# Optimization experiments

Hardware: AMD Instinct MI355X
Metric: run time of the kernel (lower is better)

The kernel has to match this reference:

```python
import jax, jax.numpy as jnp
import numpy as np

# module hyperparameters (from init_kwargs)
STRIDE, PAD, DIL = 1, 1, 1
GROUPS, DG = 1, 1
KH, KW = 3, 3
CIN, COUT = 256, 256


def _mdcn_forward(x, offset, mask, weight, bias):
    B, C, H, W = x.shape
    Cout = weight.shape[0]
    K = KH * KW
    Ho = (H + 2 * PAD - (DIL * (KH - 1) + 1)) // STRIDE + 1
    Wo = (W + 2 * PAD - (DIL * (KW - 1) + 1)) // STRIDE + 1
    Cg = C // DG

    # offset channel layout: ((g*K + k)*2 + {0: dy, 1: dx})
    off = offset.reshape(B, DG, KH, KW, 2, Ho, Wo)
    base_y = (jnp.arange(Ho) * STRIDE - PAD)[None, :] + DIL * jnp.arange(KH)[:, None]  # [KH,Ho]
    base_x = (jnp.arange(Wo) * STRIDE - PAD)[None, :] + DIL * jnp.arange(KW)[:, None]  # [KW,Wo]
    sy = base_y[None, None, :, None, :, None].astype(x.dtype) + off[:, :, :, :, 0]  # [B,DG,KH,KW,Ho,Wo]
    sx = base_x[None, None, None, :, None, :].astype(x.dtype) + off[:, :, :, :, 1]

    y0f = jnp.floor(sy); x0f = jnp.floor(sx)
    wy = sy - y0f; wx = sx - x0f
    y0 = y0f.astype(jnp.int32); x0 = x0f.astype(jnp.int32)

    xg = x.reshape(B, DG, Cg, H * W)

    def corner(yc, xc, w):
        valid = (yc >= 0) & (yc < H) & (xc >= 0) & (xc < W)
        idx = jnp.clip(yc, 0, H - 1) * W + jnp.clip(xc, 0, W - 1)  # [B,DG,KH,KW,Ho,Wo]
        v = jnp.take_along_axis(xg, idx.reshape(B, DG, 1, -1), axis=3)  # [B,DG,Cg,K*Ho*Wo]
        v = v.reshape(B, DG, Cg, KH, KW, Ho, Wo)
        return v * (w * valid.astype(x.dtype))[:, :, None]

    val = (corner(y0, x0, (1 - wy) * (1 - wx))
           + corner(y0, x0 + 1, (1 - wy) * wx)
           + corner(y0 + 1, x0, wy * (1 - wx))
           + corner(y0 + 1, x0 + 1, wy * wx))  # [B,DG,Cg,KH,KW,Ho,Wo]

    cols = val * mask.reshape(B, DG, 1, KH, KW, Ho, Wo)
    cols = cols.reshape(B, GROUPS, (C // GROUPS) * K, Ho * Wo)
    wg = weight.reshape(GROUPS, Cout // GROUPS, (C // GROUPS) * K)
    out = jnp.einsum('gok,bgkp->bgop', wg, cols).reshape(B, Cout, Ho, Wo)
    return out + bias[None, :, None, None]


def setup_inputs() -> dict:
    key = jax.random.key(0)
    k1, k2, k3, k4 = jax.random.split(key, 4)
    B, H, W = 4, 64, 64
    x = jax.random.normal(k1, (B, CIN, H, W), dtype=jnp.float32)
    offset = jax.random.normal(k2, (B, 2 * DG * KH * KW, H, W), dtype=jnp.float32)
    mask = jax.random.uniform(k3, (B, DG * KH * KW, H, W), dtype=jnp.float32)
    stdv = 1.0 / np.sqrt(CIN * KH * KW)
    weight = jax.random.uniform(k4, (COUT, CIN // GROUPS, KH, KW), dtype=jnp.float32,
                                minval=-stdv, maxval=stdv)
    bias = jnp.zeros((COUT,), dtype=jnp.float32)
    return {"x": x, "offset": offset, "mask": mask, "weight": weight, "bias": bias}


def reference(x, offset, mask, weight, bias):
    return _mdcn_forward(x, offset, mask, weight, bias)
```

## Files before the change

kernel.cpp:

```cpp
#include <hip/hip_runtime.h>
#include <hip/hip_bf16.h>
#include <stdint.h>

#define KDIM 2304

typedef __bf16 bf16_t;
typedef bf16_t bf16x8 __attribute__((ext_vector_type(8)));
typedef float f32x4 __attribute__((ext_vector_type(4)));
typedef float f32x2 __attribute__((ext_vector_type(2)));

__device__ __forceinline__ float b2f_lo(uint32_t u) {
  union { uint32_t i; float f; } c; c.i = u << 16; return c.f;
}
__device__ __forceinline__ float b2f_hi(uint32_t u) {
  union { uint32_t i; float f; } c; c.i = u & 0xffff0000u; return c.f;
}
__device__ __forceinline__ uint32_t pk_bf16(float a, float b) {
  __hip_bfloat162 h = __float22bfloat162_rn(make_float2(a, b));
  union { __hip_bfloat162 h; uint32_t u; } c; c.h = h; return c.u;
}

__device__ __forceinline__ void g2lds16(const uint16_t* g, uint16_t* l) {
  __builtin_amdgcn_global_load_lds((const __attribute__((address_space(1))) void*)g,
                                   (__attribute__((address_space(3))) void*)l,
                                   16, 0, 0);
}

__global__ __launch_bounds__(256) void k_transpose(const float* __restrict__ x,
                                                   uint16_t* __restrict__ xt) {
  __shared__ float tile[32][33];
  int b = blockIdx.z;
  int c0 = blockIdx.y << 5;
  int s0 = blockIdx.x << 5;
  int tid = threadIdx.x;
  int tx = tid & 31, ty = tid >> 5;
  const float* src = x + ((size_t)(b * 256 + c0)) * 4096 + s0;
#pragma unroll
  for (int i = 0; i < 4; ++i)
    tile[ty + i * 8][tx] = src[(size_t)(ty + i * 8) * 4096 + tx];
  __syncthreads();
  int cg = tid & 7, sp = tid >> 3;
  uint2 o;
  o.x = pk_bf16(tile[cg * 4 + 0][sp], tile[cg * 4 + 1][sp]);
  o.y = pk_bf16(tile[cg * 4 + 2][sp], tile[cg * 4 + 3][sp]);
  *(uint2*)&xt[((size_t)b * 4096 + s0 + sp) * 256 + c0 + cg * 4] = o;
}

__global__ __launch_bounds__(256) void k_wprep(const float* __restrict__ w,
                                               uint16_t* __restrict__ wt) {
  int t = blockIdx.x * 256 + threadIdx.x;
  int cout = t / KDIM;
  int r = t - cout * KDIM;
  int k = r >> 8, c = r & 255;
  wt[t] = (uint16_t)(pk_bf16(w[((size_t)(cout * 256 + c)) * 9 + k], 0.f) & 0xffffu);
}

__global__ __launch_bounds__(256) void k_im2col(const uint16_t* __restrict__ xt,
                                                const float* __restrict__ off,
                                                const float* __restrict__ msk,
                                                uint16_t* __restrict__ cols) {
  __shared__ float s_off[18 * 16];
  __shared__ float s_msk[9 * 16];
  int blk = blockIdx.x;
  int wq = blk & 3;
  int ho = (blk >> 2) & 63;
  int b = blk >> 8;
  int w0 = wq << 4;
  int tid = threadIdx.x;
  if (tid < 18 * 16) {
    int ch = tid >> 4, woi = tid & 15;
    s_off[tid] = off[((size_t)(b * 18 + ch)) * 4096 + ho * 64 + w0 + woi];
  } else if (tid >= 64 && tid < 64 + 9 * 16) {
    int i = tid - 64;
  }
  __syncthreads();
  for (int i = tid; i < 18 * 16; i += 256) {
    int ch = i >> 4, woi = i & 15;
    s_off[i] = off[((size_t)(b * 18 + ch)) * 4096 + ho * 64 + w0 + woi];
  }
  for (int i = tid; i < 9 * 16; i += 256) {
    int ch = i >> 4, woi = i & 15;
    s_msk[i] = msk[((size_t)(b * 9 + ch)) * 4096 + ho * 64 + w0 + woi];
  }
  __syncthreads();
  int wv = tid >> 6, lane = tid & 63;
  int half = lane >> 5, li = lane & 31;
  int c8 = li << 3;
  const uint16_t* base = xt + (size_t)b * 4096 * 256;
  uint16_t* cbase = cols + ((size_t)b * 4096 + (size_t)ho * 64 + w0) * KDIM;
  for (int p = wv; p < 72; p += 4) {
    int s = 2 * p + half;
    int k = s >> 4, woi = s & 15;
    int kh = k / 3, kw = k - kh * 3;
    float dy = s_off[(2 * k) * 16 + woi];
    float dx = s_off[(2 * k + 1) * 16 + woi];
    float mm = s_msk[k * 16 + woi];
    float sy = (float)(ho - 1 + kh) + dy;
    float sx = (float)(w0 + woi - 1 + kw) + dx;
    float fy = floorf(sy), fx = floorf(sx);
    int y0 = (int)fy, x0 = (int)fx;
    float wy = sy - fy, wx = sx - fx;
    f32x2 a0 = {0.f, 0.f}, a1 = {0.f, 0.f}, a2 = {0.f, 0.f}, a3 = {0.f, 0.f};
#pragma unroll
    for (int cy = 0; cy < 2; ++cy) {
#pragma unroll
      for (int cx = 0; cx < 2; ++cx) {
        int y = y0 + cy, x = x0 + cx;
        float w = (cy ? wy : 1.f - wy) * (cx ? wx : 1.f - wx);
        bool v = ((unsigned)y < 64u) && ((unsigned)x < 64u);
        w = v ? w : 0.f;
        int yc = min(max(y, 0), 63), xc = min(max(x, 0), 63);
        const uint4 d = *(const uint4*)(base + (((size_t)yc * 64 + xc) * 256 + c8));
        f32x2 ww = {w, w};
        a0 += ww * f32x2{b2f_lo(d.x), b2f_hi(d.x)};
        a1 += ww * f32x2{b2f_lo(d.y), b2f_hi(d.y)};
        a2 += ww * f32x2{b2f_lo(d.z), b2f_hi(d.z)};
        a3 += ww * f32x2{b2f_lo(d.w), b2f_hi(d.w)};
      }
    }
    f32x2 mm2 = {mm, mm};
    a0 *= mm2; a1 *= mm2; a2 *= mm2; a3 *= mm2;
    uint4 o;
    o.x = pk_bf16(a0.x, a0.y);
    o.y = pk_bf16(a1.x, a1.y);
    o.z = pk_bf16(a2.x, a2.y);
    o.w = pk_bf16(a3.x, a3.y);
    *(uint4*)(cbase + (size_t)woi * KDIM + k * 256 + c8) = o;
  }
}

#define BM 128
#define BN 64
#define BK 32
__global__ __launch_bounds__(256) void k_gemm(const uint16_t* __restrict__ A,
                                              const uint16_t* __restrict__ Bm,
                                              const float* __restrict__ bias,
                                              float* __restrict__ out) {
  __shared__ __align__(16) uint16_t As[BM * BK];
  __shared__ __align__(16) uint16_t Bs[BN * BK];
  int tid = threadIdx.x;
  int lane = tid & 63, wv = tid >> 6;
  int wm = wv >> 1, wn = wv & 1;
  int m0 = blockIdx.y * BM, n0 = blockIdx.x * BN;
  int q = lane >> 4, r = lane & 15;

  f32x4 acc[4][2];
#pragma unroll
  for (int i = 0; i < 4; ++i)
#pragma unroll
    for (int j = 0; j < 2; ++j) acc[i][j] = f32x4{0.f, 0.f, 0.f, 0.f};

  const uint16_t* a0p = A + (size_t)(m0 + (tid >> 2)) * KDIM + (tid & 3) * 8;
  const uint16_t* a1p = A + (size_t)(m0 + 64 + (tid >> 2)) * KDIM + (tid & 3) * 8;
  const uint16_t* b0p = Bm + (size_t)(n0 + (tid >> 2)) * KDIM + (tid & 3) * 8;
  uint16_t* as0 = &As[tid * 8];
  uint16_t* as1 = &As[2048 + tid * 8];
  uint16_t* bs0 = &Bs[tid * 8];

  for (int k0 = 0; k0 < KDIM; k0 += BK) {
    g2lds16(a0p + k0, as0);
    g2lds16(a1p + k0, as1);
    g2lds16(b0p + k0, bs0);
    __syncthreads();
    bf16x8 af[4], bfr[2];
#pragma unroll
    for (int mi = 0; mi < 4; ++mi)
      af[mi] = *(const bf16x8*)&As[(wm * 64 + mi * 16 + r) * BK + q * 8];
#pragma unroll
    for (int ni = 0; ni < 2; ++ni)
      bfr[ni] = *(const bf16x8*)&Bs[(wn * 32 + ni * 16 + r) * BK + q * 8];
#pragma unroll
    for (int mi = 0; mi < 4; ++mi)
#pragma unroll
      for (int ni = 0; ni < 2; ++ni)
        acc[mi][ni] = __builtin_amdgcn_mfma_f32_16x16x32_bf16(af[mi], bfr[ni], acc[mi][ni], 0, 0, 0);
    __syncthreads();
  }

#pragma unroll
  for (int mi = 0; mi < 4; ++mi) {
#pragma unroll
    for (int j = 0; j < 4; ++j) {
      int m = m0 + wm * 64 + mi * 16 + q * 4 + j;
      float bv = bias[m];
#pragma unroll
      for (int ni = 0; ni < 2; ++ni) {
        int n = n0 + wn * 32 + ni * 16 + r;
        int b = n >> 12, p = n & 4095;
        out[((size_t)(b * 256 + m)) * 4096 + p] = acc[mi][ni][j] + bv;
      }
    }
  }
}

extern "C" void kernel_launch(void* const* d_in, const int* in_sizes, int n_in,
                              void* d_out, int out_size, void* d_ws, size_t ws_size,
                              hipStream_t stream) {
  (void)in_sizes; (void)n_in; (void)out_size; (void)ws_size;
  const float* x      = (const float*)d_in[0];
  const float* offset = (const float*)d_in[1];
  const float* mask   = (const float*)d_in[2];
  const float* weight = (const float*)d_in[3];
  const float* bias   = (const float*)d_in[4];
  float* out = (float*)d_out;

  uint8_t* ws = (uint8_t*)d_ws;
  uint16_t* xt   = (uint16_t*)ws;
  uint16_t* wt   = (uint16_t*)(ws + 8388608);
  uint16_t* cols = (uint16_t*)(ws + 9568256);

  k_transpose<<<dim3(128, 8, 4), 256, 0, stream>>>(x, xt);
  k_wprep<<<dim3(2304), 256, 0, stream>>>(weight, wt);
  k_im2col<<<dim3(1024), 256, 0, stream>>>(xt, offset, mask, cols);
  k_gemm<<<dim3(256, 2), 256, 0, stream>>>(wt, cols, bias, out);
}
```

Before: 141.4 us.

## Fuse deformable im2col sampling into the GEMM B-tile loader

Removes the separate im2col kernel and its large bf16 cols buffer in global memory. Each GEMM block now computes its B tile on the fly by bilinearly sampling the channel-last input for one tap and 32 channels per K-step, with the mask folded into the corner weights. This trades the cols write and re-read traffic for redundant sampling, since each of the two M-blocks recomputes the same B tiles. It also puts gather latency inside the MFMA loop with no double buffering.

```diff
diff --git a/kernel.cpp b/kernel.cpp
--- a/kernel.cpp
+++ b/kernel.cpp
@@ -55,126 +55,127 @@
   wt[t] = (uint16_t)(pk_bf16(w[((size_t)(cout * 256 + c)) * 9 + k], 0.f) & 0xffffu);
 }
 
-__global__ __launch_bounds__(256) void k_im2col(const uint16_t* __restrict__ xt,
-                                                const float* __restrict__ off,
-                                                const float* __restrict__ msk,
-                                                uint16_t* __restrict__ cols) {
-  __shared__ float s_off[18 * 16];
-  __shared__ float s_msk[9 * 16];
-  int blk = blockIdx.x;
-  int wq = blk & 3;
-  int ho = (blk >> 2) & 63;
-  int b = blk >> 8;
-  int w0 = wq << 4;
+#define BM 128
+#define BN 64
+#define BK 32
+__global__ __launch_bounds__(256) void k_fused(const uint16_t* __restrict__ xt,
+                                               const uint16_t* __restrict__ A,
+                                               const float* __restrict__ off,
+                                               const float* __restrict__ msk,
+                                               const float* __restrict__ bias,
+                                               float* __restrict__ out) {
+  __shared__ __align__(16) uint16_t As[BM * BK];
+  __shared__ __align__(16) uint16_t Bs[BN * BK];
+  __shared__ float s_off[18 * 64];
+  __shared__ float s_msk[9 * 64];
+
   int tid = threadIdx.x;
-  if (tid < 18 * 16) {
-    int ch = tid >> 4, woi = tid & 15;
-    s_off[tid] = off[((size_t)(b * 18 + ch)) * 4096 + ho * 64 + w0 + woi];
-  } else if (tid >= 64 && tid < 64 + 9 * 16) {
-    int i = tid - 64;
-  }
+  int n0 = blockIdx.x << 6;
+  int m0 = blockIdx.y << 7;
+  int b = blockIdx.x >> 6;
+  int ho = blockIdx.x & 63;
+
+  const float* offb = off + (size_t)b * 18 * 4096 + ho * 64;
+  for (int i = tid; i < 18 * 64; i += 256)
+    s_off[i] = offb[(size_t)(i >> 6) * 4096 + (i & 63)];
+  const float* mskb = msk + (size_t)b * 9 * 4096 + ho * 64;
+  for (int i = tid; i < 9 * 64; i += 256)
+    s_msk[i] = mskb[(size_t)(i >> 6) * 4096 + (i & 63)];
   __syncthreads();
-  for (int i = tid; i < 18 * 16; i += 256) {
-    int ch = i >> 4, woi = i & 15;
-    s_off[i] = off[((size_t)(b * 18 + ch)) * 4096 + ho * 64 + w0 + woi];
-  }
-  for (int i = tid; i < 9 * 16; i += 256) {
-    int ch = i >> 4, woi = i & 15;
-    s_msk[i] = msk[((size_t)(b * 9 + ch)) * 4096 + ho * 64 + w0 + woi];
-  }
-  __syncthreads();
-  int wv = tid >> 6, lane = tid & 63;
-  int half = lane >> 5, li = lane & 31;
-  int c8 = li << 3;
-  const uint16_t* base = xt + (size_t)b * 4096 * 256;
-  uint16_t* cbase = cols + ((size_t)b * 4096 + (size_t)ho * 64 + w0) * KDIM;
-  for (int p = wv; p < 72; p += 4) {
-    int s = 2 * p + half;
-    int k = s >> 4, woi = s & 15;
-    int kh = k / 3, kw = k - kh * 3;
-    float dy = s_off[(2 * k) * 16 + woi];
-    float dx = s_off[(2 * k + 1) * 16 + woi];
-    float mm = s_msk[k * 16 + woi];
+
+  int lane = tid & 63, wv = tid >> 6;
+  int wm = wv >> 1, wn = wv & 1;
+  int q = lane >> 4, r = lane & 15;
+
+  f32x4 acc[4][2];
+#pragma unroll
+  for (int i = 0; i < 4; ++i)
+#pragma unroll
+    for (int j = 0; j < 2; ++j) acc[i][j] = f32x4{0.f, 0.f, 0.f, 0.f};
+
+  const uint16_t* a0p = A + (size_t)(m0 + (tid >> 2)) * KDIM + (tid & 3) * 8;
+  const uint16_t* a1p = A + (size_t)(m0 + 64 + (tid >> 2)) * KDIM + (tid & 3) * 8;
+  uint16_t* as0 = &As[tid * 8];
+  uint16_t* as1 = &As[2048 + tid * 8];
+
+  int p = tid >> 2, cq = tid & 3;
+  uint16_t* bs_dst = &Bs[tid * 8];
+  const uint16_t* xtb = xt + (size_t)b * 4096 * 256 + cq * 8;
+
+  for (int tap = 0; tap < 9; ++tap) {
+    int kh = tap / 3, kw = tap - kh * 3;
+    float dy = s_off[(2 * tap) * 64 + p];
+    float dx = s_off[(2 * tap + 1) * 64 + p];
+    float mm = s_msk[tap * 64 + p];
     float sy = (float)(ho - 1 + kh) + dy;
-    float sx = (float)(w0 + woi - 1 + kw) + dx;
+    float sx = (float)(p - 1 + kw) + dx;
     float fy = floorf(sy), fx = floorf(sx);
     int y0 = (int)fy, x0 = (int)fx;
     float wy = sy - fy, wx = sx - fx;
-    f32x2 a0 = {0.f, 0.f}, a1 = {0.f, 0.f}, a2 = {0.f, 0.f}, a3 = {0.f, 0.f};
+    float cw[4];
+    const uint16_t* cp[4];
 #pragma unroll
     for (int cy = 0; cy < 2; ++cy) {
 #pragma unroll
       for (int cx = 0; cx < 2; ++cx) {
         int y = y0 + cy, x = x0 + cx;
-        float w = (cy ? wy : 1.f - wy) * (cx ? wx : 1.f - wx);
+        float w = (cy ? wy : 1.f - wy) * (cx ? wx : 1.f - wx) * mm;
         bool v = ((unsigned)y < 64u) && ((unsigned)x < 64u);
         w = v ? w : 0.f;
         int yc = min(max(y, 0), 63), xc = min(max(x, 0), 63);
-        const uint4 d = *(const uint4*)(base + (((size_t)yc * 64 + xc) * 256 + c8));
-        f32x2 ww = {w, w};
-        a0 += ww * f32x2{b2f_lo(d.x), b2f_hi(d.x)};
-        a1 += ww * f32x2{b2f_lo(d.y), b2f_hi(d.y)};
-        a2 += ww * f32x2{b2f_lo(d.z), b2f_hi(d.z)};
-        a3 += ww * f32x2{b2f_lo(d.w), b2f_hi(d.w)};
+        cw[cy * 2 + cx] = w;
+        cp[cy * 2 + cx] = xtb + ((yc << 6) + xc) * 256;
       }
     }
-    f32x2 mm2 = {mm, mm};
-    a0 *= mm2; a1 *= mm2; a2 *= mm2; a3 *= mm2;
-    uint4 o;
-    o.x = pk_bf16(a0.x, a0.y);
-    o.y = pk_bf16(a1.x, a1.y);
-    o.z = pk_bf16(a2.x, a2.y);
-    o.w = pk_bf16(a3.x, a3.y);
-    *(uint4*)(cbase + (size_t)woi * KDIM + k * 256 + c8) = o;
-  }
-}
-
-#define BM 128
-#define BN 64
-#define BK 32
-__global__ __launch_bounds__(256) void k_gemm(const uint16_t* __restrict__ A,
-                                              const uint16_t* __restrict__ Bm,
-                                              const float* __restrict__ bias,
-                                              float* __restrict__ out) {
-  __shared__ __align__(16) uint16_t As[BM * BK];
-  __shared__ __align__(16) uint16_t Bs[BN * BK];
-  int tid = threadIdx.x;
-  int lane = tid & 63, wv = tid >> 6;
-  int wm = wv >> 1, wn = wv & 1;
-  int m0 = blockIdx.y * BM, n0 = blockIdx.x * BN;
-  int q = lane >> 4, r = lane & 15;
-
-  f32x4 acc[4][2];
-#pragma unroll
-  for (int i = 0; i < 4; ++i)
-#pragma unroll
-    for (int j = 0; j < 2; ++j) acc[i][j] = f32x4{0.f, 0.f, 0.f, 0.f};
-
-  const uint16_t* a0p = A + (size_t)(m0 + (tid >> 2)) * KDIM + (tid & 3) * 8;
-  const uint16_t* a1p = A + (size_t)(m0 + 64 + (tid >> 2)) * KDIM + (tid & 3) * 8;
-  const uint16_t* b0p = Bm + (size_t)(n0 + (tid >> 2)) * KDIM + (tid & 3) * 8;
-  uint16_t* as0 = &As[tid * 8];
-  uint16_t* as1 = &As[2048 + tid * 8];
-  uint16_t* bs0 = &Bs[tid * 8];
-
-  for (int k0 = 0; k0 < KDIM; k0 += BK) {
-    g2lds16(a0p + k0, as0);
-    g2lds16(a1p + k0, as1);
-    g2lds16(b0p + k0, bs0);
-    __syncthreads();
-    bf16x8 af[4], bfr[2];
-#pragma unroll
-    for (int mi = 0; mi < 4; ++mi)
-      af[mi] = *(const bf16x8*)&As[(wm * 64 + mi * 16 + r) * BK + q * 8];
-#pragma unroll
-    for (int ni = 0; ni < 2; ++ni)
-      bfr[ni] = *(const bf16x8*)&Bs[(wn * 32 + ni * 16 + r) * BK + q * 8];
-#pragma unroll
-    for (int mi = 0; mi < 4; ++mi)
+    const uint16_t* abase0 = a0p + tap * 256;
+    const uint16_t* abase1 = a1p + tap * 256;
+#pragma unroll
+    for (int st = 0; st < 8; ++st) {
+      g2lds16(abase0 + st * 32, as0);
+      g2lds16(abase1 + st * 32, as1);
+      const uint4 d0 = *(const uint4*)(cp[0] + st * 32);
+      const uint4 d1 = *(const uint4*)(cp[1] + st * 32);
+      const uint4 d2 = *(const uint4*)(cp[2] + st * 32);
+      const uint4 d3 = *(const uint4*)(cp[3] + st * 32);
+      f32x2 v0 = {0.f, 0.f}, v1 = {0.f, 0.f}, v2 = {0.f, 0.f}, v3 = {0.f, 0.f};
+      f32x2 w0 = {cw[0], cw[0]}, w1 = {cw[1], cw[1]}, w2 = {cw[2], cw[2]}, w3 = {cw[3], cw[3]};
+      v0 += w0 * f32x2{b2f_lo(d0.x), b2f_hi(d0.x)};
+      v1 += w0 * f32x2{b2f_lo(d0.y), b2f_hi(d0.y)};
+      v2 += w0 * f32x2{b2f_lo(d0.z), b2f_hi(d0.z)};
+      v3 += w0 * f32x2{b2f_lo(d0.w), b2f_hi(d0.w)};
+      v0 += w1 * f32x2{b2f_lo(d1.x), b2f_hi(d1.x)};
+      v1 += w1 * f32x2{b2f_lo(d1.y), b2f_hi(d1.y)};
+      v2 += w1 * f32x2{b2f_lo(d1.z), b2f_hi(d1.z)};
+      v3 += w1 * f32x2{b2f_lo(d1.w), b2f_hi(d1.w)};
+      v0 += w2 * f32x2{b2f_lo(d2.x), b2f_hi(d2.x)};
+      v1 += w2 * f32x2{b2f_lo(d2.y), b2f_hi(d2.y)};
+      v2 += w2 * f32x2{b2f_lo(d2.z), b2f_hi(d2.z)};
+      v3 += w2 * f32x2{b2f_lo(d2.w), b2f_hi(d2.w)};
+      v0 += w3 * f32x2{b2f_lo(d3.x), b2f_hi(d3.x)};
+      v1 += w3 * f32x2{b2f_lo(d3.y), b2f_hi(d3.y)};
+      v2 += w3 * f32x2{b2f_lo(d3.z), b2f_hi(d3.z)};
+      v3 += w3 * f32x2{b2f_lo(d3.w), b2f_hi(d3.w)};
+      uint4 o;
+      o.x = pk_bf16(v0.x, v0.y);
+      o.y = pk_bf16(v1.x, v1.y);
+      o.z = pk_bf16(v2.x, v2.y);
+      o.w = pk_bf16(v3.x, v3.y);
+      *(uint4*)bs_dst = o;
+      __syncthreads();
+      bf16x8 af[4], bfr[2];
+#pragma unroll
+      for (int mi = 0; mi < 4; ++mi)
+        af[mi] = *(const bf16x8*)&As[(wm * 64 + mi * 16 + r) * BK + q * 8];
 #pragma unroll
       for (int ni = 0; ni < 2; ++ni)
-        acc[mi][ni] = __builtin_amdgcn_mfma_f32_16x16x32_bf16(af[mi], bfr[ni], acc[mi][ni], 0, 0, 0);
-    __syncthreads();
+        bfr[ni] = *(const bf16x8*)&Bs[(wn * 32 + ni * 16 + r) * BK + q * 8];
+#pragma unroll
+      for (int mi = 0; mi < 4; ++mi)
+#pragma unroll
+        for (int ni = 0; ni < 2; ++ni)
+          acc[mi][ni] = __builtin_amdgcn_mfma_f32_16x16x32_bf16(af[mi], bfr[ni], acc[mi][ni], 0, 0, 0);
+      __syncthreads();
+    }
   }
 
 #pragma unroll
@@ -186,8 +187,8 @@
 #pragma unroll
       for (int ni = 0; ni < 2; ++ni) {
         int n = n0 + wn * 32 + ni * 16 + r;
-        int b = n >> 12, p = n & 4095;
-        out[((size_t)(b * 256 + m)) * 4096 + p] = acc[mi][ni][j] + bv;
+        int bb = n >> 12, pp = n & 4095;
+        out[((size_t)(bb * 256 + m)) * 4096 + pp] = acc[mi][ni][j] + bv;
       }
     }
   }
@@ -205,12 +206,10 @@
   float* out = (float*)d_out;
 
   uint8_t* ws = (uint8_t*)d_ws;
-  uint16_t* xt   = (uint16_t*)ws;
-  uint16_t* wt   = (uint16_t*)(ws + 8388608);
-  uint16_t* cols = (uint16_t*)(ws + 9568256);
+  uint16_t* xt = (uint16_t*)ws;
+  uint16_t* wt = (uint16_t*)(ws + 8388608);
 
   k_transpose<<<dim3(128, 8, 4), 256, 0, stream>>>(x, xt);
   k_wprep<<<dim3(2304), 256, 0, stream>>>(weight, wt);
-  k_im2col<<<dim3(1024), 256, 0, stream>>>(xt, offset, mask, cols);
-  k_gemm<<<dim3(256, 2), 256, 0, stream>>>(wt, cols, bias, out);
-}
+  k_fused<<<dim3(256, 2), 256, 0, stream>>>(xt, wt, offset, mask, bias, out);
+}
```

New measurement: 142.5 us. Within noise of the previous version (+0.8%).
